# Kernel optimization log

Measured on AMD Instinct MI355X. Metric: run time of the kernel, lower is better.

## Reference

```python
import jax, jax.numpy as jnp
import numpy as np

DIM, QK, GS, DEPTH, VOCAB, ROT = 16, 128, 256, 8, 1024, 32
EPS = 1e-5


def scale_norm(x, g):
    # ScaleNorm: x / max(||x|| * dim^-0.5, eps) * g
    norm = jnp.linalg.norm(x, axis=-1, keepdims=True) * (DIM ** -0.5)
    return x / jnp.clip(norm, EPS) * g


def rotate_half(x):
    # interleaved pairs: (x0,x1,x2,x3,...) -> (-x1,x0,-x3,x2,...)
    xr = x.reshape(x.shape[:-1] + (-1, 2))
    a, b = xr[..., 0], xr[..., 1]
    return jnp.stack((-b, a), axis=-1).reshape(x.shape)


def apply_rotary(x, cos, sin):
    # rotary applied to first ROT dims only
    xr, xp = x[..., :ROT], x[..., ROT:]
    return jnp.concatenate([xr * cos + rotate_half(xr) * sin, xp], axis=-1)


def flash_layer(x, p, cos, sin, keymask, n):
    b = x.shape[0]
    normed = scale_norm(x, p['norm_g'])
    # shift_tokens: first half of channels shifted forward by one position
    xs, xp = jnp.split(normed, 2, axis=-1)
    xs = jnp.pad(xs, ((0, 0), (1, 0), (0, 0)))[:, :-1]
    normed = jnp.concatenate([xs, xp], axis=-1)
    hid = jax.nn.silu(normed @ p['Wh'] + p['bh'])  # [b,n,64]
    v, gate = jnp.split(hid, 2, axis=-1)           # each [b,n,32]
    qk = jax.nn.silu(normed @ p['Wqk'] + p['bqk'])  # [b,n,128]
    offs = qk[..., None, :] * p['gamma'] + p['beta']  # [b,n,4,128]
    quad_q, lin_q, quad_k, lin_k = [apply_rotary(offs[..., i, :], cos, sin) for i in range(4)]
    pad = (-n) % GS
    grp = lambda t: jnp.pad(t, ((0, 0), (0, pad), (0, 0))).reshape(b, -1, GS, t.shape[-1])
    quad_q, quad_k, lin_q, lin_k, vg = map(grp, (quad_q, quad_k, lin_q, lin_k, v))
    # quadratic (local, within-group) attention with ReLU^2
    sim = jnp.einsum('bgid,bgjd->bgij', quad_q, quad_k) / GS
    attn = jnp.square(jax.nn.relu(sim)) * keymask  # mask out padded keys
    quad_out = jnp.einsum('bgij,bgjd->bgid', attn, vg)
    # linear (global, across-group) attention, reduced over groups
    lin_kv = jnp.einsum('bgnd,bgne->bde', lin_k, vg) / n
    lin_out = jnp.einsum('bgnd,bde->bgne', lin_q, lin_kv)
    out = (quad_out + lin_out).reshape(b, -1, v.shape[-1])[:, :n]
    out = gate * out
    return out @ p['Wo'] + p['bo'] + x


def forward(kmer_data, token_emb, pos_scale, norm_g, Wh, bh, Wqk, bqk, gamma, beta, Wo, bo, final_g, Wl, bl, W1, b1, W2, b2):
    b, n = kmer_data.shape
    x = token_emb[kmer_data]  # [b,n,16]
    t = jnp.arange(n, dtype=jnp.float32)
    # ScaledSinuEmbedding
    inv = 1.0 / (10000.0 ** (jnp.arange(0, DIM, 2, dtype=jnp.float32) / DIM))
    sinu = t[:, None] * inv[None, :]
    pos = jnp.concatenate([jnp.sin(sinu), jnp.cos(sinu)], axis=-1) * pos_scale
    x = x + pos
    # rotary tables (dim 32, interleaved repeat)
    rinv = 1.0 / (10000.0 ** (jnp.arange(0, ROT, 2, dtype=jnp.float32) / ROT))
    rf = jnp.repeat(t[:, None] * rinv[None, :], 2, axis=-1)  # [n,32]
    cos, sin = jnp.cos(rf), jnp.sin(rf)
    # key mask for padded positions (996 -> 1024)
    pad = (-n) % GS
    keymask = jnp.pad(jnp.ones((n,), jnp.float32), (0, pad)).reshape(1, -1, 1, GS)
    for i in range(DEPTH):
        p = dict(norm_g=norm_g[i], Wh=Wh[i], bh=bh[i], Wqk=Wqk[i], bqk=bqk[i],
                 gamma=gamma[i], beta=beta[i], Wo=Wo[i], bo=bo[i])
        x = flash_layer(x, p, cos, sin, keymask, n)
    logits = scale_norm(x, final_g) @ Wl + bl  # [b,n,1024]
    h = jnp.max(logits, axis=-1)               # AdaptiveMaxPool1d(1) + Flatten -> [b,n]
    h = jax.nn.relu(h @ W1 + b1)
    return h @ W2 + b2                          # [b,1]


def setup_inputs() -> dict:
    key = jax.random.key(0)
    ks = jax.random.split(key, 12)
    r = lambda k, shape, s: jax.random.normal(k, shape, jnp.float32) * s
    return {
        'kmer_data': jax.random.randint(ks[0], (128, 996), 0, VOCAB),
        'token_emb': r(ks[1], (VOCAB, DIM), 1.0),
        'pos_scale': jnp.float32(1.0),
        'norm_g': jnp.ones((DEPTH,), jnp.float32),
        'Wh': r(ks[2], (DEPTH, DIM, 64), 0.1),
        'bh': jnp.zeros((DEPTH, 64), jnp.float32),
        'Wqk': r(ks[3], (DEPTH, DIM, QK), 0.1),
        'bqk': jnp.zeros((DEPTH, QK), jnp.float32),
        'gamma': 1.0 + r(ks[4], (DEPTH, 4, QK), 0.02),
        'beta': r(ks[5], (DEPTH, 4, QK), 0.02),
        'Wo': r(ks[6], (DEPTH, 32, DIM), 0.1),
        'bo': jnp.zeros((DEPTH, DIM), jnp.float32),
        'final_g': jnp.float32(1.0),
        'Wl': r(ks[7], (DIM, VOCAB), 0.1),
        'bl': jnp.zeros((VOCAB,), jnp.float32),
        'W1': r(ks[8], (996, 32), 0.05),
        'b1': jnp.zeros((32,), jnp.float32),
        'W2': r(ks[9], (32, 1), 0.1),
        'b2': jnp.zeros((1,), jnp.float32),
    }


def reference(kmer_data, token_emb, pos_scale, norm_g, Wh, bh, Wqk, bqk, gamma, beta, Wo, bo, final_g, Wl, bl, W1, b1, W2, b2):
    return forward(kmer_data, token_emb, pos_scale, norm_g, Wh, bh, Wqk, bqk,
                   gamma, beta, Wo, bo, final_g, Wl, bl, W1, b1, W2, b2)
```

## Files before the change

### kernel.cpp

```cpp
#include <hip/hip_runtime.h>

typedef short s16x8 __attribute__((ext_vector_type(8)));
typedef float f32x4 __attribute__((ext_vector_type(4)));

#define NB    128
#define NTOK  996
#define NPAD  1024
#define NGRP  4
#define GSZ   256
#define NLAY  8

__device__ __forceinline__ float bf2f(unsigned short u){
    unsigned int v = ((unsigned int)u) << 16;
    return __uint_as_float(v);
}
__device__ __forceinline__ unsigned short f2bf(float f){
    unsigned int x = __float_as_uint(f);
    unsigned int r = (x + 0x7fffu + ((x >> 16) & 1u)) >> 16;
    return (unsigned short)r;
}
__device__ __forceinline__ unsigned int packbf(float a, float b){
    return (unsigned int)f2bf(a) | ((unsigned int)f2bf(b) << 16);
}
__device__ __forceinline__ float silu(float v){
    return v / (1.0f + __expf(-v));
}

__device__ __forceinline__ s16x8 derive_core(const unsigned short* __restrict__ qrow, int d0,
        float4 g0, float4 g1, float4 b0, float4 b1,
        const float* __restrict__ rp, bool rot){
    uint4 u = *(const uint4*)(qrow + d0);
    float y0 = bf2f((unsigned short)(u.x & 0xffffu))*g0.x + b0.x;
    float y1 = bf2f((unsigned short)(u.x >> 16))    *g0.y + b0.y;
    float y2 = bf2f((unsigned short)(u.y & 0xffffu))*g0.z + b0.z;
    float y3 = bf2f((unsigned short)(u.y >> 16))    *g0.w + b0.w;
    float y4 = bf2f((unsigned short)(u.z & 0xffffu))*g1.x + b1.x;
    float y5 = bf2f((unsigned short)(u.z >> 16))    *g1.y + b1.y;
    float y6 = bf2f((unsigned short)(u.w & 0xffffu))*g1.z + b1.z;
    float y7 = bf2f((unsigned short)(u.w >> 16))    *g1.w + b1.w;
    if (rot){
        float4 c4 = *(const float4*)(rp);
        float4 s4 = *(const float4*)(rp + 16);
        float a;
        a = y0; y0 = a*c4.x - y1*s4.x; y1 = y1*c4.x + a*s4.x;
        a = y2; y2 = a*c4.y - y3*s4.y; y3 = y3*c4.y + a*s4.y;
        a = y4; y4 = a*c4.z - y5*s4.z; y5 = y5*c4.z + a*s4.z;
        a = y6; y6 = a*c4.w - y7*s4.w; y7 = y7*c4.w + a*s4.w;
    }
    union { unsigned int uu[4]; s16x8 s; } r;
    r.uu[0] = packbf(y0, y1);
    r.uu[1] = packbf(y2, y3);
    r.uu[2] = packbf(y4, y5);
    r.uu[3] = packbf(y6, y7);
    return r.s;
}

__global__ void k_rope(float* __restrict__ rope){
    int t = blockIdx.x * 256 + threadIdx.x;
    if (t >= NPAD) return;
    float tf = (float)t;
    #pragma unroll
    for (int i = 0; i < 16; i++){
        float inv = expf(((float)(2*i) / 32.0f) * -9.210340371976184f);
        float ang = tf * inv;
        rope[t*32 + i]      = cosf(ang);
        rope[t*32 + 16 + i] = sinf(ang);
    }
}

__global__ __launch_bounds__(256) void k_embed(const int* __restrict__ kmer,
                                               const float* __restrict__ emb,
                                               const float* __restrict__ ps,
                                               float* __restrict__ x){
    int gid = blockIdx.x * 256 + threadIdx.x;
    if (gid >= NB * NTOK) return;
    int b = gid / NTOK;
    int tt = gid - b * NTOK;
    int idx = kmer[gid];
    const float* er = emb + (size_t)idx * 16;
    float pscale = ps[0];
    float tf = (float)tt;
    float* xr = x + (size_t)gid * 16;
    #pragma unroll
    for (int i = 0; i < 8; i++){
        float inv = expf(((float)(2*i) / 16.0f) * -9.210340371976184f);
        float ang = tf * inv;
        xr[i]     = er[i]     + sinf(ang) * pscale;
        xr[8 + i] = er[8 + i] + cosf(ang) * pscale;
    }
}

__global__ __launch_bounds__(256) void k_padzero(unsigned short* __restrict__ vT){
    int rid = blockIdx.x * 256 + threadIdx.x;
    if (rid < NB * 32){
        unsigned int* vp = (unsigned int*)(vT + (size_t)rid * NPAD + NTOK);
        #pragma unroll
        for (int i = 0; i < 14; i++) vp[i] = 0u;
    }
}

__global__ __launch_bounds__(256) void k_pre(const float* __restrict__ x,
                                             const float* __restrict__ Wh, const float* __restrict__ bh,
                                             const float* __restrict__ Wqk, const float* __restrict__ bqk,
                                             const float* __restrict__ norm_g, int layer,
                                             unsigned short* __restrict__ qk,
                                             unsigned short* __restrict__ vT,
                                             unsigned short* __restrict__ gateb){
    __shared__ __align__(16) unsigned short WcT[192 * 40];
    __shared__ __align__(16) unsigned short As[256 * 40];
    __shared__ unsigned int nrm[256][4];
    int tid = threadIdx.x;
    const float* Whl = Wh  + (size_t)layer * 1024;
    const float* Wql = Wqk + (size_t)layer * 2048;
    for (int i = tid; i < 1024; i += 256){ int d = i >> 6, c = i & 63;  WcT[c*40 + d] = f2bf(Whl[i]); }
    for (int i = tid; i < 2048; i += 256){ int d = i >> 7, c = i & 127; WcT[(64 + c)*40 + d] = f2bf(Wql[i]); }
    if (tid < 192){
        int i = tid;
        float bv = (i < 64) ? bh[layer*64 + i] : bqk[layer*128 + (i - 64)];
        WcT[i*40 + 16] = f2bf(bv);
        WcT[i*40 + 17] = 0;
        unsigned int* zz = (unsigned int*)(WcT + i*40 + 18);
        #pragma unroll
        for (int k = 0; k < 7; k++) zz[k] = 0u;
    }
    int gid0 = blockIdx.x * 256;
    int t = gid0 + tid;
    int b = t / NTOK, tt = t - b * NTOK;
    float g = norm_g[layer];
    unsigned int* dd = (unsigned int*)(As + tid * 40);
    {
        const float4* xr4 = (const float4*)(x + (size_t)t * 16);
        float cur[16];
        float s2 = 0.f;
        #pragma unroll
        for (int c = 0; c < 4; c++){
            float4 v4 = xr4[c];
            cur[4*c] = v4.x; cur[4*c+1] = v4.y; cur[4*c+2] = v4.z; cur[4*c+3] = v4.w;
        }
        #pragma unroll
        for (int d = 0; d < 16; d++) s2 += cur[d]*cur[d];
        float sc = g / fmaxf(sqrtf(s2) * 0.25f, 1e-5f);
        #pragma unroll
        for (int i = 0; i < 4; i++) nrm[tid][i] = packbf(cur[2*i]*sc, cur[2*i+1]*sc);
        #pragma unroll
        for (int i = 0; i < 4; i++) dd[4 + i] = packbf(cur[8 + 2*i]*sc, cur[9 + 2*i]*sc);
        dd[8] = 0x00003f80u;
        #pragma unroll
        for (int i = 9; i < 16; i++) dd[i] = 0u;
    }
    __syncthreads();
    if (tt == 0){
        #pragma unroll
        for (int i = 0; i < 4; i++) dd[i] = 0u;
    } else if (tid > 0){
        #pragma unroll
        for (int i = 0; i < 4; i++) dd[i] = nrm[tid - 1][i];
    } else {
        const float4* xp4 = (const float4*)(x + (size_t)(t - 1) * 16);
        float prv[16]; float p2 = 0.f;
        #pragma unroll
        for (int c = 0; c < 4; c++){
            float4 v4 = xp4[c];
            prv[4*c] = v4.x; prv[4*c+1] = v4.y; prv[4*c+2] = v4.z; prv[4*c+3] = v4.w;
        }
        #pragma unroll
        for (int d = 0; d < 16; d++) p2 += prv[d]*prv[d];
        float sp = g / fmaxf(sqrtf(p2) * 0.25f, 1e-5f);
        #pragma unroll
        for (int i = 0; i < 4; i++) dd[i] = packbf(prv[2*i]*sp, prv[2*i+1]*sp);
    }
    __syncthreads();
    int w = tid >> 6, lane = tid & 63, m16 = lane & 15, quad = lane >> 4;
    s16x8 wf[12];
    #pragma unroll
    for (int mi = 0; mi < 12; mi++)
        wf[mi] = *(const s16x8*)(WcT + (mi*16 + m16)*40 + quad*8);
    f32x4 zacc = {0.f,0.f,0.f,0.f};
    #pragma unroll
    for (int nt = 0; nt < 4; nt++){
        int tloc = w*64 + nt*16 + m16;
        int tg = gid0 + tloc;
        int bb = tg / NTOK, ttt = tg - bb * NTOK;
        s16x8 bf = *(const s16x8*)(As + tloc*40 + quad*8);
        size_t rowq = ((size_t)bb*NPAD + ttt);
        #pragma unroll
        for (int mi = 0; mi < 12; mi++){
            f32x4 r = __builtin_amdgcn_mfma_f32_16x16x32_bf16(wf[mi], bf, zacc, 0, 0, 0);
            float sv[4];
            #pragma unroll
            for (int reg = 0; reg < 4; reg++) sv[reg] = silu(r[reg]);
            int wc0 = mi*16 + quad*4;
            if (mi < 2){
                #pragma unroll
                for (int reg = 0; reg < 4; reg++)
                    vT[((size_t)bb*32 + wc0 + reg)*NPAD + ttt] = f2bf(sv[reg]);
            } else if (mi < 4){
                *(uint2*)(gateb + rowq*32 + (wc0 - 32)) = make_uint2(packbf(sv[0],sv[1]), packbf(sv[2],sv[3]));
            } else {
                *(uint2*)(qk + rowq*128 + (wc0 - 64)) = make_uint2(packbf(sv[0],sv[1]), packbf(sv[2],sv[3]));
            }
        }
    }
}

__global__ __launch_bounds__(256) void k_linkv(const unsigned short* __restrict__ qk,
                                               const unsigned short* __restrict__ vT,
                                               const float* __restrict__ rope,
                                               const float* __restrict__ gamma, const float* __restrict__ beta,
                                               int layer, float* __restrict__ linkvp){
    __shared__ __align__(16) unsigned short LkT[2][128 * 40];
    int tid = threadIdx.x;
    int b = blockIdx.x >> 2, qt = blockIdx.x & 3;
    const float* gam = gamma + (size_t)layer * 512 + 384;
    const float* bet = beta  + (size_t)layer * 512 + 384;
    int tt = tid >> 3, dseg = (tid & 7) * 16;
    float gr[16], br[16];
    #pragma unroll
    for (int i = 0; i < 16; i++){ gr[i] = gam[dseg + i]; br[i] = bet[dseg + i]; }
    int w = tid >> 6, lane = tid & 63, m16 = lane & 15, quad = lane >> 4;
    f32x4 acc[2][2] = {{{0,0,0,0},{0,0,0,0}},{{0,0,0,0},{0,0,0,0}}};
    for (int ch = 0; ch < 8; ch++){
        unsigned short* L = LkT[ch & 1];
        {
            int t = qt*256 + ch*32 + tt;
            const uint4* s4 = (const uint4*)(qk + ((size_t)b * NPAD + t) * 128 + dseg);
            float y[16];
            #pragma unroll
            for (int c = 0; c < 2; c++){
                uint4 u = s4[c];
                unsigned int uu[4] = {u.x, u.y, u.z, u.w};
                #pragma unroll
                for (int k = 0; k < 4; k++){
                    int dl = c*8 + 2*k;
                    y[dl]   = bf2f((unsigned short)(uu[k] & 0xffffu)) * gr[dl]   + br[dl];
                    y[dl+1] = bf2f((unsigned short)(uu[k] >> 16))     * gr[dl+1] + br[dl+1];
                }
            }
            if (dseg < 32){
                const float* rp = rope + t*32 + (dseg >> 1);
                #pragma unroll
                for (int i = 0; i < 8; i++){
                    float c = rp[i], s = rp[16 + i];
                    float ya = y[2*i], yb = y[2*i+1];
                    y[2*i]   = ya*c - yb*s;
                    y[2*i+1] = yb*c + ya*s;
                }
            }
            #pragma unroll
            for (int i = 0; i < 16; i++) L[(dseg + i)*40 + tt] = f2bf(y[i]);
        }
        __syncthreads();
        int t0 = qt*256 + ch*32;
        s16x8 af0 = *(const s16x8*)(L + ((w*2)  *16 + m16)*40 + quad*8);
        s16x8 af1 = *(const s16x8*)(L + ((w*2+1)*16 + m16)*40 + quad*8);
        s16x8 bf0 = *(const s16x8*)(vT + ((size_t)b*32 + m16)*NPAD + t0 + quad*8);
        s16x8 bf1 = *(const s16x8*)(vT + ((size_t)b*32 + 16 + m16)*NPAD + t0 + quad*8);
        acc[0][0] = __builtin_amdgcn_mfma_f32_16x16x32_bf16(af0, bf0, acc[0][0], 0,0,0);
        acc[0][1] = __builtin_amdgcn_mfma_f32_16x16x32_bf16(af0, bf1, acc[0][1], 0,0,0);
        acc[1][0] = __builtin_amdgcn_mfma_f32_16x16x32_bf16(af1, bf0, acc[1][0], 0,0,0);
        acc[1][1] = __builtin_amdgcn_mfma_f32_16x16x32_bf16(af1, bf1, acc[1][1], 0,0,0);
    }
    const float invn = 1.0f / 996.0f;
    #pragma unroll
    for (int i = 0; i < 2; i++){
        #pragma unroll
        for (int j = 0; j < 2; j++){
            int e = j*16 + m16;
            #pragma unroll
            for (int reg = 0; reg < 4; reg++){
                int d = (w*2 + i)*16 + quad*4 + reg;
                linkvp[(((size_t)qt*NB + b)*32 + e)*128 + d] = acc[i][j][reg] * invn;
            }
        }
    }
}

#define KD_BYTES (64*136*2)
#define PW_BYTES (8*16*72*2)
__global__ __launch_bounds__(512, 2) void k_quad(const unsigned short* __restrict__ qk,
                                              const unsigned short* __restrict__ vT,
                                              const unsigned short* __restrict__ gateb,
                                              const float* __restrict__ linkvp,
                                              const float* __restrict__ rope,
                                              const float* __restrict__ gamma, const float* __restrict__ beta,
                                              int layer,
                                              const float* __restrict__ Wo, const float* __restrict__ bo,
                                              float* __restrict__ x){
    __shared__ __align__(16) unsigned char smem[KD_BYTES + PW_BYTES];
    __shared__ __align__(16) unsigned short LkBs[32 * 136];
    __shared__ float sWo[512];
    __shared__ float sbo[16];
    unsigned short* Kd = (unsigned short*)smem;
    unsigned short* Pw = (unsigned short*)(smem + KD_BYTES);
    int tid = threadIdx.x;
    int blk = blockIdx.x;
    int g = blk & 3, b = blk >> 2;
    int tg0 = g * GSZ;
    const float* gamL = gamma + (size_t)layer * 512;
    const float* betL = beta  + (size_t)layer * 512;
    sWo[tid] = Wo[layer*512 + tid];
    if (tid < 16) sbo[tid] = bo[layer*16 + tid];

    int w = tid >> 6, lane = tid & 63, m16 = lane & 15, quad = lane >> 4;

    int tqA = tg0 + w*32 + m16;
    int tqB = tqA + 16;
    const unsigned short* qrowA = qk + ((size_t)b*NPAD + tqA)*128;
    const unsigned short* qrowB = qk + ((size_t)b*NPAD + tqB)*128;
    const float* rpA = rope + tqA*32 + quad*4;
    const float* rpB = rope + tqB*32 + quad*4;
    s16x8 qf[2][4];
    #pragma unroll
    for (int ks = 0; ks < 4; ks++){
        int d0 = ks*32 + quad*8;
        float4 g0 = *(const float4*)(gamL + d0), g1 = *(const float4*)(gamL + d0 + 4);
        float4 b0 = *(const float4*)(betL + d0), b1 = *(const float4*)(betL + d0 + 4);
        bool rot = (ks == 0) && (quad < 4);
        qf[0][ks] = derive_core(qrowA, d0, g0,g1,b0,b1, rpA, rot);
        qf[1][ks] = derive_core(qrowB, d0, g0,g1,b0,b1, rpB, rot);
    }

    const float* gK = gamL + 256;
    const float* bK = betL + 256;
    f32x4 oacc[2][2] = {{{0,0,0,0},{0,0,0,0}},{{0,0,0,0},{0,0,0,0}}};
    unsigned short* myP = Pw + w*16*72;

    for (int ch = 0; ch < 4; ch++){
        __syncthreads();
        {
            int r = tid >> 3, seg = (tid & 7) * 16;
            int tk = tg0 + ch*64 + r;
            const unsigned short* krow = qk + ((size_t)b*NPAD + tk)*128 + seg;
            unsigned int* dst = (unsigned int*)(Kd + r*136 + seg);
            #pragma unroll
            for (int h = 0; h < 2; h++){
                uint4 u = ((const uint4*)krow)[h];
                unsigned int uu[4] = {u.x, u.y, u.z, u.w};
                float y[8];
                #pragma unroll
                for (int k = 0; k < 4; k++){
                    int d = h*8 + 2*k;
                    y[2*k]   = bf2f((unsigned short)(uu[k] & 0xffffu)) * gK[seg + d]     + bK[seg + d];
                    y[2*k+1] = bf2f((unsigned short)(uu[k] >> 16))     * gK[seg + d + 1] + bK[seg + d + 1];
                }
                if (seg < 32){
                    const float* rp = rope + tk*32 + (seg >> 1) + h*4;
                    #pragma unroll
                    for (int p = 0; p < 4; p++){
                        float c = rp[p], s = rp[16 + p];
                        float a = y[2*p], d = y[2*p+1];
                        y[2*p]   = a*c - d*s;
                        y[2*p+1] = d*c + a*s;
                    }
                }
                #pragma unroll
                for (int k = 0; k < 4; k++) dst[h*4 + k] = packbf(y[2*k], y[2*k+1]);
            }
        }
        __syncthreads();
        #pragma unroll
        for (int i = 0; i < 2; i++){
            #pragma unroll
            for (int np = 0; np < 2; np++){
                f32x4 s0 = {0,0,0,0}, s1 = {0,0,0,0};
                #pragma unroll
                for (int ks = 0; ks < 4; ks++){
                    s16x8 kf0 = *(const s16x8*)(Kd + ((np*2  )*16 + m16)*136 + ks*32 + quad*8);
                    s16x8 kf1 = *(const s16x8*)(Kd + ((np*2+1)*16 + m16)*136 + ks*32 + quad*8);
                    s0 = __builtin_amdgcn_mfma_f32_16x16x32_bf16(qf[i][ks], kf0, s0, 0,0,0);
                    s1 = __builtin_amdgcn_mfma_f32_16x16x32_bf16(qf[i][ks], kf1, s1, 0,0,0);
                }
                #pragma unroll
                for (int j = 0; j < 2; j++){
                    int kl = (np*2 + j)*16 + m16;
                    bool kv = (tg0 + ch*64 + kl) < NTOK;
                    #pragma unroll
                    for (int reg = 0; reg < 4; reg++){
                        float a = fmaxf(j ? s1[reg] : s0[reg], 0.0f);
                        a = a * a;
                        myP[(quad*4 + reg)*72 + kl] = kv ? f2bf(a) : (unsigned short)0;
                    }
                }
            }
            #pragma unroll
            for (int ks = 0; ks < 2; ks++){
                s16x8 pa = *(const s16x8*)(myP + m16*72 + ks*32 + quad*8);
                s16x8 vf0 = *(const s16x8*)(vT + ((size_t)b*32 + m16)*NPAD + tg0 + ch*64 + ks*32 + quad*8);
                s16x8 vf1 = *(const s16x8*)(vT + ((size_t)b*32 + 16 + m16)*NPAD + tg0 + ch*64 + ks*32 + quad*8);
                oacc[i][0] = __builtin_amdgcn_mfma_f32_16x16x32_bf16(pa, vf0, oacc[i][0], 0,0,0);
                oacc[i][1] = __builtin_amdgcn_mfma_f32_16x16x32_bf16(pa, vf1, oacc[i][1], 0,0,0);
            }
        }
    }
    const float qsc = 1.0f / 65536.0f;
    #pragma unroll
    for (int i = 0; i < 2; i++)
        #pragma unroll
        for (int j = 0; j < 2; j++)
            oacc[i][j] = oacc[i][j] * qsc;
    {
        int e = tid >> 4, dbase = (tid & 15) * 8;
        float s[8];
        #pragma unroll
        for (int k = 0; k < 8; k++) s[k] = 0.f;
        #pragma unroll
        for (int part = 0; part < 4; part++){
            const float* src = linkvp + (((size_t)part*NB + b)*32 + e)*128 + dbase;
            float4 u0 = *(const float4*)src;
            float4 u1 = *(const float4*)(src + 4);
            s[0]+=u0.x; s[1]+=u0.y; s[2]+=u0.z; s[3]+=u0.w;
            s[4]+=u1.x; s[5]+=u1.y; s[6]+=u1.z; s[7]+=u1.w;
        }
        unsigned int* dst = (unsigned int*)(LkBs + e*136 + dbase);
        #pragma unroll
        for (int k = 0; k < 4; k++) dst[k] = packbf(s[2*k], s[2*k+1]);
    }
    __syncthreads();
    {
        const float* gamQ = gamL + 128;
        const float* betQ = betL + 128;
        #pragma unroll
        for (int ks = 0; ks < 4; ks++){
            int d0 = ks*32 + quad*8;
            float4 g0 = *(const float4*)(gamQ + d0), g1 = *(const float4*)(gamQ + d0 + 4);
            float4 b0 = *(const float4*)(betQ + d0), b1 = *(const float4*)(betQ + d0 + 4);
            bool rot = (ks == 0) && (quad < 4);
            s16x8 lf0 = derive_core(qrowA, d0, g0,g1,b0,b1, rpA, rot);
            s16x8 lf1 = derive_core(qrowB, d0, g0,g1,b0,b1, rpB, rot);
            #pragma unroll
            for (int j = 0; j < 2; j++){
                s16x8 lb = *(const s16x8*)(LkBs + (j*16 + m16)*136 + ks*32 + quad*8);
                oacc[0][j] = __builtin_amdgcn_mfma_f32_16x16x32_bf16(lf0, lb, oacc[0][j], 0,0,0);
                oacc[1][j] = __builtin_amdgcn_mfma_f32_16x16x32_bf16(lf1, lb, oacc[1][j], 0,0,0);
            }
        }
    }
    float* Obw = (float*)smem + w*1056;
    #pragma unroll
    for (int i = 0; i < 2; i++)
        #pragma unroll
        for (int j = 0; j < 2; j++)
            #pragma unroll
            for (int reg = 0; reg < 4; reg++)
                Obw[(i*16 + quad*4 + reg)*33 + j*16 + m16] = oacc[i][j][reg];
    {
        int r = lane >> 1, dp = (lane & 1) * 8;
        int p = tg0 + w*32 + r;
        if (p < NTOK){
            const unsigned short* gr = gateb + ((size_t)b*NPAD + p)*32;
            float* xr = x + ((size_t)b * NTOK + p)*16 + dp;
            float4 x0 = *(const float4*)xr;
            float4 x1 = *(const float4*)(xr + 4);
            float a[8] = { sbo[dp]+x0.x, sbo[dp+1]+x0.y, sbo[dp+2]+x0.z, sbo[dp+3]+x0.w,
                           sbo[dp+4]+x1.x, sbo[dp+5]+x1.y, sbo[dp+6]+x1.z, sbo[dp+7]+x1.w };
            #pragma unroll
            for (int eh = 0; eh < 4; eh++){
                uint4 gu = *(const uint4*)(gr + eh*8);
                unsigned int gg[4] = {gu.x, gu.y, gu.z, gu.w};
                #pragma unroll
                for (int k = 0; k < 4; k++){
                    float gv0 = bf2f((unsigned short)(gg[k] & 0xffffu));
                    float gv1 = bf2f((unsigned short)(gg[k] >> 16));
                    int e = eh*8 + 2*k;
                    float ov0 = Obw[r*33 + e] * gv0;
                    float ov1 = Obw[r*33 + e + 1] * gv1;
                    const float* wr0 = &sWo[e*16 + dp];
                    const float* wr1 = &sWo[(e+1)*16 + dp];
                    #pragma unroll
                    for (int kk = 0; kk < 8; kk++) a[kk] += ov0 * wr0[kk] + ov1 * wr1[kk];
                }
            }
            *(float4*)xr = make_float4(a[0],a[1],a[2],a[3]);
            *(float4*)(xr+4) = make_float4(a[4],a[5],a[6],a[7]);
        }
    }
}

__global__ __launch_bounds__(256) void k_head(const float* __restrict__ x,
                                              const float* __restrict__ Wl, const float* __restrict__ bl,
                                              const float* __restrict__ fg, float* __restrict__ h){
    __shared__ __align__(16) unsigned short WlT[512 * 40];
    __shared__ __align__(16) unsigned short As[64 * 40];
    int tid = threadIdx.x;
    int gid0 = blockIdx.x * 64;
    if (tid < 64){
        int t = gid0 + tid;
        const float4* xr4 = (const float4*)(x + (size_t)t * 16);
        float cur[16]; float s2 = 0.f;
        #pragma unroll
        for (int c = 0; c < 4; c++){
            float4 v4 = xr4[c];
            cur[4*c] = v4.x; cur[4*c+1] = v4.y; cur[4*c+2] = v4.z; cur[4*c+3] = v4.w;
        }
        #pragma unroll
        for (int d = 0; d < 16; d++) s2 += cur[d]*cur[d];
        float sc = fg[0] / fmaxf(sqrtf(s2) * 0.25f, 1e-5f);
        unsigned int* dd = (unsigned int*)(As + tid * 40);
        #pragma unroll
        for (int i = 0; i < 8; i++) dd[i] = packbf(cur[2*i]*sc, cur[2*i+1]*sc);
        dd[8] = 0x00003f80u;
        #pragma unroll
        for (int i = 9; i < 16; i++) dd[i] = 0u;
    }
    int w = tid >> 6, lane = tid & 63, m16 = lane & 15, quad = lane >> 4;
    float vm0 = -3e38f, vm1 = -3e38f, vm2 = -3e38f, vm3 = -3e38f;
    for (int half = 0; half < 2; half++){
        __syncthreads();
        for (int i = tid; i < 8192; i += 256){
            int d = i >> 9, c = i & 511;
            WlT[c*40 + d] = f2bf(Wl[(size_t)d*1024 + half*512 + c]);
        }
        for (int i = tid; i < 512; i += 256){
            WlT[i*40 + 16] = f2bf(bl[half*512 + i]);
            WlT[i*40 + 17] = 0;
            unsigned int* zz = (unsigned int*)(WlT + i*40 + 18);
            #pragma unroll
            for (int k = 0; k < 7; k++) zz[k] = 0u;
        }
        __syncthreads();
        s16x8 af = *(const s16x8*)(As + (w*16 + m16)*40 + quad*8);
        f32x4 zacc = {0,0,0,0};
        for (int nt = 0; nt < 32; nt++){
            s16x8 bf = *(const s16x8*)(WlT + (nt*16 + m16)*40 + quad*8);
            f32x4 r = __builtin_amdgcn_mfma_f32_16x16x32_bf16(af, bf, zacc, 0,0,0);
            vm0 = fmaxf(vm0, r[0]);
            vm1 = fmaxf(vm1, r[1]);
            vm2 = fmaxf(vm2, r[2]);
            vm3 = fmaxf(vm3, r[3]);
        }
    }
    #pragma unroll
    for (int off = 1; off < 16; off <<= 1){
        vm0 = fmaxf(vm0, __shfl_xor(vm0, off, 64));
        vm1 = fmaxf(vm1, __shfl_xor(vm1, off, 64));
        vm2 = fmaxf(vm2, __shfl_xor(vm2, off, 64));
        vm3 = fmaxf(vm3, __shfl_xor(vm3, off, 64));
    }
    if (m16 == 0){
        int t0 = gid0 + w*16 + quad*4;
        h[t0 + 0] = vm0;
        h[t0 + 1] = vm1;
        h[t0 + 2] = vm2;
        h[t0 + 3] = vm3;
    }
}

__global__ __launch_bounds__(256) void k_final(const float* __restrict__ h,
                                               const float* __restrict__ W1, const float* __restrict__ b1,
                                               const float* __restrict__ W2, const float* __restrict__ b2,
                                               float* __restrict__ out){
    int b = blockIdx.x;
    int tid = threadIdx.x;
    int j = tid & 31, part = tid >> 5;
    float acc = 0.f;
    for (int i = part; i < NTOK; i += 8)
        acc += h[(size_t)b*NTOK + i] * W1[(size_t)i*32 + j];
    __shared__ float red[8][33];
    red[part][j] = acc;
    __syncthreads();
    if (tid < 32){
        float s = b1[tid];
        #pragma unroll
        for (int p = 0; p < 8; p++) s += red[p][tid];
        s = fmaxf(s, 0.f);
        red[0][tid] = s * W2[tid];
    }
    __syncthreads();
    if (tid == 0){
        float s = b2[0];
        #pragma unroll
        for (int jj = 0; jj < 32; jj++) s += red[0][jj];
        out[b] = s;
    }
}

extern "C" void kernel_launch(void* const* d_in, const int* in_sizes, int n_in,
                              void* d_out, int out_size, void* d_ws, size_t ws_size,
                              hipStream_t stream){
    const int*   kmer  = (const int*)d_in[0];
    const float* emb   = (const float*)d_in[1];
    const float* ps    = (const float*)d_in[2];
    const float* ng    = (const float*)d_in[3];
    const float* Wh    = (const float*)d_in[4];
    const float* bh    = (const float*)d_in[5];
    const float* Wqk   = (const float*)d_in[6];
    const float* bqk   = (const float*)d_in[7];
    const float* gamma = (const float*)d_in[8];
    const float* beta  = (const float*)d_in[9];
    const float* Wo    = (const float*)d_in[10];
    const float* bo    = (const float*)d_in[11];
    const float* fg    = (const float*)d_in[12];
    const float* Wl    = (const float*)d_in[13];
    const float* bl    = (const float*)d_in[14];
    const float* W1    = (const float*)d_in[15];
    const float* b1    = (const float*)d_in[16];
    const float* W2    = (const float*)d_in[17];
    const float* b2    = (const float*)d_in[18];
    float* out = (float*)d_out;

    char* wsp = (char*)d_ws;
    float* x = (float*)wsp;                     wsp += (size_t)NB*NTOK*16*4;
    unsigned short* qk = (unsigned short*)wsp;  wsp += (size_t)NB*NPAD*128*2;
    unsigned short* vT = (unsigned short*)wsp;  wsp += (size_t)NB*32*NPAD*2;
    unsigned short* gateb = (unsigned short*)wsp; wsp += (size_t)NB*NPAD*32*2;
    float* linkvp = (float*)wsp;                wsp += (size_t)4*NB*32*128*4;
    float* rope = (float*)wsp;                  wsp += (size_t)NPAD*32*4;
    float* h = (float*)wsp;                     wsp += (size_t)NB*NTOK*4;

    k_rope<<<4, 256, 0, stream>>>(rope);
    k_embed<<<(NB*NTOK + 255)/256, 256, 0, stream>>>(kmer, emb, ps, x);
    k_padzero<<<16, 256, 0, stream>>>(vT);
    for (int layer = 0; layer < NLAY; layer++){
        k_pre<<<NB*NTOK/256, 256, 0, stream>>>(x, Wh, bh, Wqk, bqk, ng, layer, qk, vT, gateb);
        k_linkv<<<NB*4, 256, 0, stream>>>(qk, vT, rope, gamma, beta, layer, linkvp);
        k_quad<<<NB*NGRP, 512, 0, stream>>>(qk, vT, gateb, linkvp, rope, gamma, beta, layer, Wo, bo, x);
    }
    k_head<<<NB*NTOK/64, 256, 0, stream>>>(x, Wl, bl, fg, h);
    k_final<<<NB, 256, 0, stream>>>(h, W1, b1, W2, b2, out);
}
```

Baseline: 912.0 us.

## Fuse linear-attention KV reduction into pre-projection kernel per batch-quarter tile

The pre-projection kernel is remapped to one block per (batch, 256-token quarter), padded to NPAD, so each block owns a contiguous token range. It then applies the lin_k gamma/beta and rotary transform in registers, stages lin_k and v transposed in shared memory, and computes the partial lin_kv product with MFMA directly. This removes the separate k_linkv and k_padzero launches and the reread of qk/vT from global memory. In exchange it raises shared memory and register use per block and adds in-loop barriers.

After: 811.9 us. -11.0%, faster.

```diff
diff --git a/kernel.cpp b/kernel.cpp
--- a/kernel.cpp
+++ b/kernel.cpp
@@ -90,28 +90,27 @@
     }
 }
 
-__global__ __launch_bounds__(256) void k_padzero(unsigned short* __restrict__ vT){
-    int rid = blockIdx.x * 256 + threadIdx.x;
-    if (rid < NB * 32){
-        unsigned int* vp = (unsigned int*)(vT + (size_t)rid * NPAD + NTOK);
-        #pragma unroll
-        for (int i = 0; i < 14; i++) vp[i] = 0u;
-    }
-}
-
-__global__ __launch_bounds__(256) void k_pre(const float* __restrict__ x,
+__global__ __launch_bounds__(256, 2) void k_pre(const float* __restrict__ x,
                                              const float* __restrict__ Wh, const float* __restrict__ bh,
                                              const float* __restrict__ Wqk, const float* __restrict__ bqk,
-                                             const float* __restrict__ norm_g, int layer,
+                                             const float* __restrict__ norm_g,
+                                             const float* __restrict__ gamma, const float* __restrict__ beta,
+                                             const float* __restrict__ rope, int layer,
                                              unsigned short* __restrict__ qk,
                                              unsigned short* __restrict__ vT,
-                                             unsigned short* __restrict__ gateb){
+                                             unsigned short* __restrict__ gateb,
+                                             float* __restrict__ linkvp){
     __shared__ __align__(16) unsigned short WcT[192 * 40];
     __shared__ __align__(16) unsigned short As[256 * 40];
     __shared__ unsigned int nrm[256][4];
+    __shared__ __align__(16) unsigned short LkT[128 * 72];
+    __shared__ __align__(16) unsigned short Vt[32 * 72];
     int tid = threadIdx.x;
+    int qt = blockIdx.x & 3, b = blockIdx.x >> 2;
     const float* Whl = Wh  + (size_t)layer * 1024;
     const float* Wql = Wqk + (size_t)layer * 2048;
+    const float* gLin = gamma + (size_t)layer * 512 + 384;
+    const float* bLin = beta  + (size_t)layer * 512 + 384;
     for (int i = tid; i < 1024; i += 256){ int d = i >> 6, c = i & 63;  WcT[c*40 + d] = f2bf(Whl[i]); }
     for (int i = tid; i < 2048; i += 256){ int d = i >> 7, c = i & 127; WcT[(64 + c)*40 + d] = f2bf(Wql[i]); }
     if (tid < 192){
@@ -123,13 +122,12 @@
         #pragma unroll
         for (int k = 0; k < 7; k++) zz[k] = 0u;
     }
-    int gid0 = blockIdx.x * 256;
-    int t = gid0 + tid;
-    int b = t / NTOK, tt = t - b * NTOK;
+    int tt = qt*256 + tid;
+    int tsafe = tt < NTOK ? tt : (NTOK - 1);
     float g = norm_g[layer];
     unsigned int* dd = (unsigned int*)(As + tid * 40);
     {
-        const float4* xr4 = (const float4*)(x + (size_t)t * 16);
+        const float4* xr4 = (const float4*)(x + ((size_t)b*NTOK + tsafe) * 16);
         float cur[16];
         float s2 = 0.f;
         #pragma unroll
@@ -156,7 +154,7 @@
         #pragma unroll
         for (int i = 0; i < 4; i++) dd[i] = nrm[tid - 1][i];
     } else {
-        const float4* xp4 = (const float4*)(x + (size_t)(t - 1) * 16);
+        const float4* xp4 = (const float4*)(x + ((size_t)b*NTOK + tt - 1) * 16);
         float prv[16]; float p2 = 0.f;
         #pragma unroll
         for (int c = 0; c < 4; c++){
@@ -176,13 +174,15 @@
     for (int mi = 0; mi < 12; mi++)
         wf[mi] = *(const s16x8*)(WcT + (mi*16 + m16)*40 + quad*8);
     f32x4 zacc = {0.f,0.f,0.f,0.f};
+    f32x4 lacc[2][2] = {{{0,0,0,0},{0,0,0,0}},{{0,0,0,0},{0,0,0,0}}};
     #pragma unroll
     for (int nt = 0; nt < 4; nt++){
         int tloc = w*64 + nt*16 + m16;
-        int tg = gid0 + tloc;
-        int bb = tg / NTOK, ttt = tg - bb * NTOK;
+        int ttk = qt*256 + tloc;
+        bool tv = ttk < NTOK;
+        int c = w*16 + m16;
         s16x8 bf = *(const s16x8*)(As + tloc*40 + quad*8);
-        size_t rowq = ((size_t)bb*NPAD + ttt);
+        size_t rowq = ((size_t)b*NPAD + ttk);
         #pragma unroll
         for (int mi = 0; mi < 12; mi++){
             f32x4 r = __builtin_amdgcn_mfma_f32_16x16x32_bf16(wf[mi], bf, zacc, 0, 0, 0);
@@ -192,73 +192,46 @@
             int wc0 = mi*16 + quad*4;
             if (mi < 2){
                 #pragma unroll
-                for (int reg = 0; reg < 4; reg++)
-                    vT[((size_t)bb*32 + wc0 + reg)*NPAD + ttt] = f2bf(sv[reg]);
+                for (int reg = 0; reg < 4; reg++){
+                    unsigned short pv = tv ? f2bf(sv[reg]) : (unsigned short)0;
+                    vT[((size_t)b*32 + wc0 + reg)*NPAD + ttk] = pv;
+                    Vt[(wc0 + reg)*72 + c] = pv;
+                }
             } else if (mi < 4){
                 *(uint2*)(gateb + rowq*32 + (wc0 - 32)) = make_uint2(packbf(sv[0],sv[1]), packbf(sv[2],sv[3]));
             } else {
-                *(uint2*)(qk + rowq*128 + (wc0 - 64)) = make_uint2(packbf(sv[0],sv[1]), packbf(sv[2],sv[3]));
-            }
-        }
-    }
-}
-
-__global__ __launch_bounds__(256) void k_linkv(const unsigned short* __restrict__ qk,
-                                               const unsigned short* __restrict__ vT,
-                                               const float* __restrict__ rope,
-                                               const float* __restrict__ gamma, const float* __restrict__ beta,
-                                               int layer, float* __restrict__ linkvp){
-    __shared__ __align__(16) unsigned short LkT[2][128 * 40];
-    int tid = threadIdx.x;
-    int b = blockIdx.x >> 2, qt = blockIdx.x & 3;
-    const float* gam = gamma + (size_t)layer * 512 + 384;
-    const float* bet = beta  + (size_t)layer * 512 + 384;
-    int tt = tid >> 3, dseg = (tid & 7) * 16;
-    float gr[16], br[16];
-    #pragma unroll
-    for (int i = 0; i < 16; i++){ gr[i] = gam[dseg + i]; br[i] = bet[dseg + i]; }
-    int w = tid >> 6, lane = tid & 63, m16 = lane & 15, quad = lane >> 4;
-    f32x4 acc[2][2] = {{{0,0,0,0},{0,0,0,0}},{{0,0,0,0},{0,0,0,0}}};
-    for (int ch = 0; ch < 8; ch++){
-        unsigned short* L = LkT[ch & 1];
-        {
-            int t = qt*256 + ch*32 + tt;
-            const uint4* s4 = (const uint4*)(qk + ((size_t)b * NPAD + t) * 128 + dseg);
-            float y[16];
-            #pragma unroll
-            for (int c = 0; c < 2; c++){
-                uint4 u = s4[c];
-                unsigned int uu[4] = {u.x, u.y, u.z, u.w};
-                #pragma unroll
-                for (int k = 0; k < 4; k++){
-                    int dl = c*8 + 2*k;
-                    y[dl]   = bf2f((unsigned short)(uu[k] & 0xffffu)) * gr[dl]   + br[dl];
-                    y[dl+1] = bf2f((unsigned short)(uu[k] >> 16))     * gr[dl+1] + br[dl+1];
-                }
-            }
-            if (dseg < 32){
-                const float* rp = rope + t*32 + (dseg >> 1);
-                #pragma unroll
-                for (int i = 0; i < 8; i++){
-                    float c = rp[i], s = rp[16 + i];
-                    float ya = y[2*i], yb = y[2*i+1];
-                    y[2*i]   = ya*c - yb*s;
-                    y[2*i+1] = yb*c + ya*s;
-                }
-            }
-            #pragma unroll
-            for (int i = 0; i < 16; i++) L[(dseg + i)*40 + tt] = f2bf(y[i]);
+                int qd = wc0 - 64;
+                *(uint2*)(qk + rowq*128 + qd) = make_uint2(packbf(sv[0],sv[1]), packbf(sv[2],sv[3]));
+                float y0 = sv[0]*gLin[qd]   + bLin[qd];
+                float y1 = sv[1]*gLin[qd+1] + bLin[qd+1];
+                float y2 = sv[2]*gLin[qd+2] + bLin[qd+2];
+                float y3 = sv[3]*gLin[qd+3] + bLin[qd+3];
+                if (qd < 32){
+                    const float* rp = rope + ttk*32 + (qd >> 1);
+                    float c0 = rp[0], s0 = rp[16], c1 = rp[1], s1 = rp[17];
+                    float a;
+                    a = y0; y0 = a*c0 - y1*s0; y1 = y1*c0 + a*s0;
+                    a = y2; y2 = a*c1 - y3*s1; y3 = y3*c1 + a*s1;
+                }
+                LkT[(qd+0)*72 + c] = f2bf(y0);
+                LkT[(qd+1)*72 + c] = f2bf(y1);
+                LkT[(qd+2)*72 + c] = f2bf(y2);
+                LkT[(qd+3)*72 + c] = f2bf(y3);
+            }
         }
         __syncthreads();
-        int t0 = qt*256 + ch*32;
-        s16x8 af0 = *(const s16x8*)(L + ((w*2)  *16 + m16)*40 + quad*8);
-        s16x8 af1 = *(const s16x8*)(L + ((w*2+1)*16 + m16)*40 + quad*8);
-        s16x8 bf0 = *(const s16x8*)(vT + ((size_t)b*32 + m16)*NPAD + t0 + quad*8);
-        s16x8 bf1 = *(const s16x8*)(vT + ((size_t)b*32 + 16 + m16)*NPAD + t0 + quad*8);
-        acc[0][0] = __builtin_amdgcn_mfma_f32_16x16x32_bf16(af0, bf0, acc[0][0], 0,0,0);
-        acc[0][1] = __builtin_amdgcn_mfma_f32_16x16x32_bf16(af0, bf1, acc[0][1], 0,0,0);
-        acc[1][0] = __builtin_amdgcn_mfma_f32_16x16x32_bf16(af1, bf0, acc[1][0], 0,0,0);
-        acc[1][1] = __builtin_amdgcn_mfma_f32_16x16x32_bf16(af1, bf1, acc[1][1], 0,0,0);
+        #pragma unroll
+        for (int ks2 = 0; ks2 < 2; ks2++){
+            s16x8 a0 = *(const s16x8*)(LkT + ((2*w  )*16 + m16)*72 + ks2*32 + quad*8);
+            s16x8 a1 = *(const s16x8*)(LkT + ((2*w+1)*16 + m16)*72 + ks2*32 + quad*8);
+            s16x8 b0 = *(const s16x8*)(Vt + (m16)*72 + ks2*32 + quad*8);
+            s16x8 b1 = *(const s16x8*)(Vt + (16 + m16)*72 + ks2*32 + quad*8);
+            lacc[0][0] = __builtin_amdgcn_mfma_f32_16x16x32_bf16(a0, b0, lacc[0][0], 0,0,0);
+            lacc[0][1] = __builtin_amdgcn_mfma_f32_16x16x32_bf16(a0, b1, lacc[0][1], 0,0,0);
+            lacc[1][0] = __builtin_amdgcn_mfma_f32_16x16x32_bf16(a1, b0, lacc[1][0], 0,0,0);
+            lacc[1][1] = __builtin_amdgcn_mfma_f32_16x16x32_bf16(a1, b1, lacc[1][1], 0,0,0);
+        }
+        __syncthreads();
     }
     const float invn = 1.0f / 996.0f;
     #pragma unroll
@@ -268,8 +241,8 @@
             int e = j*16 + m16;
             #pragma unroll
             for (int reg = 0; reg < 4; reg++){
-                int d = (w*2 + i)*16 + quad*4 + reg;
-                linkvp[(((size_t)qt*NB + b)*32 + e)*128 + d] = acc[i][j][reg] * invn;
+                int d = (2*w + i)*16 + quad*4 + reg;
+                linkvp[(((size_t)qt*NB + b)*32 + e)*128 + d] = lacc[i][j][reg] * invn;
             }
         }
     }
@@ -609,10 +582,8 @@
 
     k_rope<<<4, 256, 0, stream>>>(rope);
     k_embed<<<(NB*NTOK + 255)/256, 256, 0, stream>>>(kmer, emb, ps, x);
-    k_padzero<<<16, 256, 0, stream>>>(vT);
     for (int layer = 0; layer < NLAY; layer++){
-        k_pre<<<NB*NTOK/256, 256, 0, stream>>>(x, Wh, bh, Wqk, bqk, ng, layer, qk, vT, gateb);
-        k_linkv<<<NB*4, 256, 0, stream>>>(qk, vT, rope, gamma, beta, layer, linkvp);
+        k_pre<<<NB*4, 256, 0, stream>>>(x, Wh, bh, Wqk, bqk, ng, gamma, beta, rope, layer, qk, vT, gateb, linkvp);
         k_quad<<<NB*NGRP, 512, 0, stream>>>(qk, vT, gateb, linkvp, rope, gamma, beta, layer, Wo, bo, x);
     }
     k_head<<<NB*NTOK/64, 256, 0, stream>>>(x, Wl, bl, fg, h);
```
